# Optimization experiments

Measured on AMD Instinct MI355X. Metric: run time of the kernel, lower is better.

## Reference

```python
import jax, jax.numpy as jnp
import numpy as np

N_NODES = 50000
N_EDGES = 600000
IN_DIM = 128
HID = 128


def gcn_conv(x, W, b, src, dst, num_nodes):
    """PyG-style GCNConv: add self-loops, symmetric D^-1/2 (A+I) D^-1/2 normalization."""
    xw = x @ W  # [N, H]
    loop = jnp.arange(num_nodes)
    s = jnp.concatenate([src, loop])
    d = jnp.concatenate([dst, loop])
    deg = jax.ops.segment_sum(jnp.ones_like(d, dtype=xw.dtype), d, num_segments=num_nodes)
    dinv = jax.lax.rsqrt(deg)  # deg >= 1 thanks to self-loops
    norm = dinv[s] * dinv[d]  # [E+N]
    msgs = xw[s] * norm[:, None]  # gather + scale, [E+N, H]
    out = jax.ops.segment_sum(msgs, d, num_segments=num_nodes)
    return out + b


def setup_inputs() -> dict:
    key = jax.random.key(0)
    ks = jax.random.split(key, 12)
    sc_in = 1.0 / np.sqrt(IN_DIM)
    sc_h = 1.0 / np.sqrt(HID)
    sc_2h = 1.0 / np.sqrt(2 * HID)
    return {
        "x": jax.random.normal(ks[0], (N_NODES, IN_DIM), jnp.float32),
        "hidden_state": jax.random.normal(ks[1], (N_NODES, HID), jnp.float32),
        "edge_index": jax.random.randint(ks[2], (2, N_EDGES), 0, N_NODES, dtype=jnp.int32),
        "W_in": jax.random.normal(ks[3], (IN_DIM, HID), jnp.float32) * sc_in,
        "b_in": jnp.zeros((HID,), jnp.float32),
        "W_hid": jax.random.normal(ks[4], (HID, HID), jnp.float32) * sc_h,
        "b_hid": jnp.zeros((HID,), jnp.float32),
        "W_z": jax.random.normal(ks[5], (2 * HID, HID), jnp.float32) * sc_2h,
        "b_z": jnp.zeros((HID,), jnp.float32),
        "W_r": jax.random.normal(ks[6], (2 * HID, HID), jnp.float32) * sc_2h,
        "b_r": jnp.zeros((HID,), jnp.float32),
        "W_c": jax.random.normal(ks[7], (2 * HID, HID), jnp.float32) * sc_2h,
        "b_c": jnp.zeros((HID,), jnp.float32),
    }


def reference(x, hidden_state, edge_index, W_in, b_in, W_hid, b_hid, W_z, b_z, W_r, b_r, W_c, b_c):
    src, dst = edge_index[0], edge_index[1]
    n = x.shape[0]
    # two stacked GCN layers (dropout identity in eval mode)
    h1 = jax.nn.relu(gcn_conv(x, W_in, b_in, src, dst, n))
    emb = gcn_conv(h1, W_hid, b_hid, src, dst, n)  # [N, H]
    # GRU-style gating
    combined = jnp.concatenate([emb, hidden_state], axis=1)  # [N, 2H]
    update = jax.nn.sigmoid(combined @ W_z + b_z)
    reset = jax.nn.sigmoid(combined @ W_r + b_r)
    cand_in = jnp.concatenate([emb, reset * hidden_state], axis=1)
    candidate = jnp.tanh(cand_in @ W_c + b_c)
    new_hidden = (1.0 - update) * hidden_state + update * candidate
    return new_hidden
```

## Files before the change

kernel.cpp:

```cpp
#include <hip/hip_runtime.h>
#include <cstdint>
#include <cstddef>

typedef unsigned short u16;
typedef unsigned int   u32;

typedef __bf16 bf8   __attribute__((ext_vector_type(8)));
typedef float  f32x4 __attribute__((ext_vector_type(4)));

__device__ __forceinline__ float b2f(u16 v) {
  union { u32 i; float f; } c; c.i = ((u32)v) << 16; return c.f;
}
__device__ __forceinline__ u16 f2b(float f) {
  union { u32 i; float f; } c; c.f = f;
  u32 x = c.i;
  u32 r = (x + 0x7FFFu + ((x >> 16) & 1u)) >> 16;
  return (u16)r;
}
__device__ __forceinline__ float sigf(float x) { return 1.0f / (1.0f + __expf(-x)); }
__device__ __forceinline__ float tanhfast(float x) { return 2.0f * sigf(2.0f * x) - 1.0f; }

__device__ __forceinline__ bf8 cvt8(const float* __restrict__ p) {
  f32x4 lo = *(const f32x4*)p;
  f32x4 hi = *(const f32x4*)(p + 4);
  union { u16 s[8]; bf8 v; } c;
#pragma unroll
  for (int i = 0; i < 4; ++i) { c.s[i] = f2b(lo[i]); c.s[4 + i] = f2b(hi[i]); }
  return c.v;
}

__device__ __forceinline__ void ld_lds16(const u16* g, u16* l) {
  __builtin_amdgcn_global_load_lds((const __attribute__((address_space(1))) void*)g,
                                   (__attribute__((address_space(3))) void*)l, 16, 0, 0);
}

#define CSR_STRIDE 80

__global__ __launch_bounds__(256) void k_transpose(
    const float* __restrict__ W0, const float* __restrict__ W1,
    const float* __restrict__ W2, const float* __restrict__ W3,
    const float* __restrict__ W4,
    u16* __restrict__ B0, u16* __restrict__ B1, u16* __restrict__ B2,
    u16* __restrict__ B3, u16* __restrict__ B4,
    int* __restrict__ cnt, int N) {
  if (blockIdx.x >= 64) {
    int i = (blockIdx.x - 64) * 256 + threadIdx.x;
    if (i < N) cnt[i] = 0;
    return;
  }
  int t = blockIdx.x * 256 + threadIdx.x;
  const float* in; u16* out; int f;
  if (t < 2048)       { in = W0; out = B0; f = t; }
  else if (t < 4096)  { in = W1; out = B1; f = t - 2048; }
  else if (t < 8192)  { in = W2; out = B2; f = t - 4096; }
  else if (t < 12288) { in = W3; out = B3; f = t - 8192; }
  else                { in = W4; out = B4; f = t - 12288; }
  int ln = f & 15, quad = (f >> 4) & 3, c = (f >> 6) & 7, ks = (f >> 9) & 3, hh = f >> 11;
  int n = c * 16 + ln;
  int k0 = hh * 128 + ks * 32 + quad * 8;
  union { u16 s[8]; uint4 q; } tmp;
#pragma unroll
  for (int j = 0; j < 8; ++j) tmp.s[j] = f2b(in[(size_t)(k0 + j) * 128 + n]);
  *(uint4*)(out + (size_t)f * 8) = tmp.q;
}

__global__ void k_fill(const int* __restrict__ src, const int* __restrict__ dst,
                       int* __restrict__ cnt, int* __restrict__ csr, int E) {
  int e = blockIdx.x * 256 + threadIdx.x;
  if (e < E) {
    int d = dst[e];
    int pos = atomicAdd(&cnt[d], 1);
    if (pos < CSR_STRIDE) csr[(size_t)d * CSR_STRIDE + pos] = src[e];
  }
}

__global__ __launch_bounds__(256) void k_agg(const u16* __restrict__ y,
                                             const int* __restrict__ cnt,
                                             const int* __restrict__ csr,
                                             const float* __restrict__ bias,
                                             u16* __restrict__ out, int relu, int N) {
  int wv = (blockIdx.x * 256 + threadIdx.x) >> 6;
  int lane = threadIdx.x & 63;
  if (wv >= N) return;
  int g = lane >> 4, t = lane & 15;
  const uint4* yq = (const uint4*)y;
  int deg = cnt[wv];
  int degc = (deg < 64) ? deg : 64;
  long base = (long)wv * CSR_STRIDE;
  int myidx = (lane < degc) ? csr[base + lane] : 0;

  float a[8];
#pragma unroll
  for (int j = 0; j < 8; ++j) a[j] = 0.0f;

  for (int b = 0; b < degc; b += 8) {
    int e0 = b + g, e1 = b + 4 + g;
    int s0 = __shfl(myidx, (e0 < degc) ? e0 : 0, 64);
    int s1 = __shfl(myidx, (e1 < degc) ? e1 : 0, 64);
    uint4 v0 = yq[(size_t)s0 * 16 + t];
    uint4 v1 = yq[(size_t)s1 * 16 + t];
    if (e0 < degc) {
      const u32* w = (const u32*)&v0;
#pragma unroll
      for (int i = 0; i < 4; ++i) { a[2*i] += b2f((u16)(w[i] & 0xFFFF)); a[2*i+1] += b2f((u16)(w[i] >> 16)); }
    }
    if (e1 < degc) {
      const u32* w = (const u32*)&v1;
#pragma unroll
      for (int i = 0; i < 4; ++i) { a[2*i] += b2f((u16)(w[i] & 0xFFFF)); a[2*i+1] += b2f((u16)(w[i] >> 16)); }
    }
  }
#pragma unroll
  for (int j = 0; j < 8; ++j) {
    a[j] += __shfl_xor(a[j], 16, 64);
    a[j] += __shfl_xor(a[j], 32, 64);
  }
  if (g == 0) {
    int degt = (deg < CSR_STRIDE) ? deg : CSR_STRIDE;
    for (int p = 64; p < degt; ++p) {
      int s = csr[base + p];
      uint4 v = yq[(size_t)s * 16 + t];
      const u32* w = (const u32*)&v;
#pragma unroll
      for (int i = 0; i < 4; ++i) { a[2*i] += b2f((u16)(w[i] & 0xFFFF)); a[2*i+1] += b2f((u16)(w[i] >> 16)); }
    }
    uint4 sv = yq[(size_t)wv * 16 + t];
    const u32* w = (const u32*)&sv;
#pragma unroll
    for (int i = 0; i < 4; ++i) { a[2*i] += b2f((u16)(w[i] & 0xFFFF)); a[2*i+1] += b2f((u16)(w[i] >> 16)); }
    float di = rsqrtf((float)deg + 1.0f);
    f32x4 b0 = *(const f32x4*)(bias + t * 8);
    f32x4 b1 = *(const f32x4*)(bias + t * 8 + 4);
    union { u16 s[8]; uint4 q; } o;
#pragma unroll
    for (int j = 0; j < 8; ++j) {
      float r = di * a[j] + ((j < 4) ? b0[j] : b1[j - 4]);
      if (relu) r = fmaxf(r, 0.0f);
      o.s[j] = f2b(r);
    }
    ((uint4*)out)[(size_t)wv * 16 + t] = o.q;
  }
}

template <bool AF>
__global__ __launch_bounds__(256) void k_gemm(
    const void* __restrict__ Av,
    const u16* __restrict__ Bt,
    const int* __restrict__ cnt,
    u16* __restrict__ outb, int M) {
  __shared__ __align__(16) u16 bs[16384];
  int tid = threadIdx.x;
  int lane = tid & 63, wave = tid >> 6;
  int ln = lane & 15, quad = lane >> 4;
  int rowbase = blockIdx.x * 64 + wave * 16;
  int rowA = rowbase + ln;
  long rA = (rowA < M) ? rowA : (M - 1);

  {
    const u16* g = Bt + wave * 4096 + lane * 8;
    u16* l = bs + wave * 4096;
#pragma unroll
    for (int i = 0; i < 8; ++i) ld_lds16(g + i * 512, l + i * 512);
  }

  bf8 af[4];
#pragma unroll
  for (int ks = 0; ks < 4; ++ks) {
    int kk = ks * 32 + quad * 8;
    if (AF) af[ks] = cvt8((const float*)Av + rA * 128 + kk);
    else    af[ks] = *(const bf8*)((const u16*)Av + rA * 128 + kk);
  }

  f32x4 acc[8];
#pragma unroll
  for (int c = 0; c < 8; ++c) { acc[c][0] = 0.f; acc[c][1] = 0.f; acc[c][2] = 0.f; acc[c][3] = 0.f; }

  __syncthreads();
#pragma unroll
  for (int ks = 0; ks < 4; ++ks) {
#pragma unroll
    for (int c = 0; c < 8; ++c) {
      bf8 bfr = *(const bf8*)(bs + ks * 4096 + c * 512 + lane * 8);
      acc[c] = __builtin_amdgcn_mfma_f32_16x16x32_bf16(af[ks], bfr, acc[c], 0, 0, 0);
    }
  }

  int rb = rowbase + quad * 4;
  float rs[4];
#pragma unroll
  for (int r = 0; r < 4; ++r) {
    int row = rb + r;
    rs[r] = (row < M) ? rsqrtf((float)cnt[row] + 1.0f) : 0.0f;
  }
#pragma unroll
  for (int c = 0; c < 8; ++c) {
    int col = c * 16 + ln;
#pragma unroll
    for (int r = 0; r < 4; ++r) {
      int row = rb + r;
      if (row < M) outb[(size_t)row * 128 + col] = f2b(acc[c][r] * rs[r]);
    }
  }
}

__global__ __launch_bounds__(256, 2) void k_gru(
    const u16* __restrict__ emb, const float* __restrict__ h,
    const u16* __restrict__ Btz, const u16* __restrict__ Btr, const u16* __restrict__ Btc,
    const float* __restrict__ bz, const float* __restrict__ br, const float* __restrict__ bc,
    float* __restrict__ out, int M) {
  __shared__ __align__(16) u16 lds[32768];
  u16* const at = lds + 24576;
  int tid = threadIdx.x;
  int lane = tid & 63, wave = tid >> 6;
  int ln = lane & 15, quad = lane >> 4;
  int rowbase = blockIdx.x * 64 + wave * 16;
  int rowA = rowbase + ln;
  long rA = (rowA < M) ? rowA : (M - 1);
  int rb = rowbase + quad * 4;

  auto stage_zr = [&](int k, int s) {
#pragma unroll
    for (int i = 0; i < 2; ++i) {
      int off = (wave * 2 + i) * 512;
      ld_lds16(Btz + k * 4096 + off + lane * 8, &lds[s * 8192 + off]);
      ld_lds16(Btr + k * 4096 + off + lane * 8, &lds[s * 8192 + 4096 + off]);
    }
  };
  auto stage_c = [&](int k, int s) {
#pragma unroll
    for (int i = 0; i < 2; ++i) {
      int off = (wave * 2 + i) * 512;
      ld_lds16(Btc + k * 4096 + off + lane * 8, &lds[s * 4096 + off]);
    }
  };

  stage_zr(0, 0);
  stage_zr(1, 1);

  bf8 af_e[4], af_h[4];
#pragma unroll
  for (int ks = 0; ks < 4; ++ks)
    af_e[ks] = *(const bf8*)(emb + rA * 128 + ks * 32 + quad * 8);
#pragma unroll
  for (int ks = 0; ks < 4; ++ks)
    af_h[ks] = cvt8(h + rA * 128 + ks * 32 + quad * 8);

  f32x4 accz[8], accr[8];
#pragma unroll
  for (int c = 0; c < 8; ++c) {
    accz[c][0] = 0.f; accz[c][1] = 0.f; accz[c][2] = 0.f; accz[c][3] = 0.f;
    accr[c][0] = 0.f; accr[c][1] = 0.f; accr[c][2] = 0.f; accr[c][3] = 0.f;
  }

#pragma unroll
  for (int k = 0; k < 8; ++k) {
    if (k < 7) asm volatile("s_waitcnt vmcnt(4)\n\ts_barrier" ::: "memory");
    else       asm volatile("s_waitcnt vmcnt(0)\n\ts_barrier" ::: "memory");
    if (k < 6) stage_zr(k + 2, (k + 2) % 3);
    bf8 af = (k < 4) ? af_e[k] : af_h[k - 4];
    int s = k % 3;
#pragma unroll
    for (int c = 0; c < 8; ++c) {
      bf8 bz_ = *(const bf8*)(&lds[s * 8192 + (c * 64 + lane) * 8]);
      bf8 br_ = *(const bf8*)(&lds[s * 8192 + 4096 + (c * 64 + lane) * 8]);
      accz[c] = __builtin_amdgcn_mfma_f32_16x16x32_bf16(af, bz_, accz[c], 0, 0, 0);
      accr[c] = __builtin_amdgcn_mfma_f32_16x16x32_bf16(af, br_, accr[c], 0, 0, 0);
    }
  }

  stage_c(0, 0);
  stage_c(1, 1);

  f32x4 hc[8];
#pragma unroll
  for (int c = 0; c < 8; ++c) {
    int col = c * 16 + ln;
#pragma unroll
    for (int r = 0; r < 4; ++r) {
      int row = rb + r;
      hc[c][r] = (row < M) ? h[(size_t)row * 128 + col] : 0.0f;
    }
  }

#pragma unroll
  for (int c = 0; c < 8; ++c) {
    int col = c * 16 + ln;
    float bzc = bz[col], brc = br[col];
#pragma unroll
    for (int r = 0; r < 4; ++r) {
      float uu = sigf(accz[c][r] + bzc);
      float rr = sigf(accr[c][r] + brc);
      accz[c][r] = uu;
      int lrow = wave * 16 + quad * 4 + r;
      at[lrow * 128 + col] = f2b(rr * hc[c][r]);
      accr[c][r] = 0.0f;
    }
  }
  __syncthreads();

  bf8 af_at[4];
#pragma unroll
  for (int ks = 0; ks < 4; ++ks)
    af_at[ks] = *(const bf8*)(at + (wave * 16 + ln) * 128 + ks * 32 + quad * 8);

#pragma unroll
  for (int j = 0; j < 8; ++j) {
    if (j < 7) asm volatile("s_waitcnt vmcnt(2)\n\ts_barrier" ::: "memory");
    else       asm volatile("s_waitcnt vmcnt(0)\n\ts_barrier" ::: "memory");
    if (j < 6) stage_c(j + 2, (j + 2) % 3);
    bf8 af = (j < 4) ? af_e[j] : af_at[j - 4];
    int s = j % 3;
#pragma unroll
    for (int c = 0; c < 8; ++c) {
      bf8 bfr = *(const bf8*)(&lds[s * 4096 + (c * 64 + lane) * 8]);
      accr[c] = __builtin_amdgcn_mfma_f32_16x16x32_bf16(af, bfr, accr[c], 0, 0, 0);
    }
  }

#pragma unroll
  for (int c = 0; c < 8; ++c) {
    int col = c * 16 + ln;
    float bcc = bc[col];
#pragma unroll
    for (int r = 0; r < 4; ++r) {
      int row = rb + r;
      if (row < M) {
        float cd = tanhfast(accr[c][r] + bcc);
        float uu = accz[c][r];
        out[(size_t)row * 128 + col] = (1.0f - uu) * hc[c][r] + uu * cd;
      }
    }
  }
}

extern "C" void kernel_launch(void* const* d_in, const int* in_sizes, int n_in,
                              void* d_out, int out_size, void* d_ws, size_t ws_size,
                              hipStream_t stream) {
  const float* x     = (const float*)d_in[0];
  const float* h     = (const float*)d_in[1];
  const int*   ei    = (const int*)d_in[2];
  const float* W_in  = (const float*)d_in[3];
  const float* b_in  = (const float*)d_in[4];
  const float* W_hid = (const float*)d_in[5];
  const float* b_hid = (const float*)d_in[6];
  const float* W_z   = (const float*)d_in[7];
  const float* b_z   = (const float*)d_in[8];
  const float* W_r   = (const float*)d_in[9];
  const float* b_r   = (const float*)d_in[10];
  const float* W_c   = (const float*)d_in[11];
  const float* b_c   = (const float*)d_in[12];

  const int N = in_sizes[0] / 128;
  const int E = in_sizes[2] / 2;
  const int* src = ei;
  const int* dst = ei + E;

  char* p = (char*)d_ws;
  auto carve = [&](size_t bytes) { char* r = p; p += (bytes + 255) & ~(size_t)255; return r; };
  u16* Bt_in   = (u16*)carve((size_t)16384 * 2);
  u16* Bt_hid  = (u16*)carve((size_t)16384 * 2);
  u16* Bt_z    = (u16*)carve((size_t)32768 * 2);
  u16* Bt_r    = (u16*)carve((size_t)32768 * 2);
  u16* Bt_c    = (u16*)carve((size_t)32768 * 2);
  int* cnt  = (int*)carve((size_t)N * 4);
  int* csr  = (int*)carve((size_t)N * CSR_STRIDE * 4);
  u16* y    = (u16*)carve((size_t)N * 128 * 2);
  u16* h1   = (u16*)carve((size_t)N * 128 * 2);
  u16* emb  = (u16*)carve((size_t)N * 128 * 2);

  int gN = (N + 255) / 256;
  int gE = (E + 255) / 256;
  int gG = (N + 63) / 64;
  int gA = (N + 3) / 4;

  k_transpose<<<64 + gN, 256, 0, stream>>>(W_in, W_hid, W_z, W_r, W_c,
                                           Bt_in, Bt_hid, Bt_z, Bt_r, Bt_c, cnt, N);
  k_fill<<<gE, 256, 0, stream>>>(src, dst, cnt, csr, E);

  k_gemm<true><<<gG, 256, 0, stream>>>(x, Bt_in, cnt, y, N);
  k_agg<<<gA, 256, 0, stream>>>(y, cnt, csr, b_in, h1, 1, N);
  k_gemm<false><<<gG, 256, 0, stream>>>(h1, Bt_hid, cnt, y, N);
  k_agg<<<gA, 256, 0, stream>>>(y, cnt, csr, b_hid, emb, 0, N);
  k_gru<<<gG, 256, 0, stream>>>(emb, h, Bt_z, Bt_r, Bt_c, b_z, b_r, b_c, (float*)d_out, N);
}
```

Baseline: 255.5 us.

## Process 32 rows per wave in GRU kernel to reuse staged weights

Each wave in the GRU kernel now handles two 16-row fragments, so each 128-row block reuses every weight tile staged in LDS across twice as many MFMAs and the grid is halved. The reset-times-hidden tile is now written to a per-wave LDS region with an XOR swizzle, which removes the block-wide __syncthreads and avoids bank conflicts. The hidden state is re-read from global memory instead of being held in registers. Together these double accumulator registers and raise LDS use, which may lower occupancy under the 256,2 launch bounds.

```diff
diff --git a/kernel.cpp b/kernel.cpp
--- a/kernel.cpp
+++ b/kernel.cpp
@@ -208,15 +208,12 @@
     const u16* __restrict__ Btz, const u16* __restrict__ Btr, const u16* __restrict__ Btc,
     const float* __restrict__ bz, const float* __restrict__ br, const float* __restrict__ bc,
     float* __restrict__ out, int M) {
-  __shared__ __align__(16) u16 lds[32768];
-  u16* const at = lds + 24576;
+  __shared__ __align__(16) u16 lds[40960];
   int tid = threadIdx.x;
   int lane = tid & 63, wave = tid >> 6;
   int ln = lane & 15, quad = lane >> 4;
-  int rowbase = blockIdx.x * 64 + wave * 16;
-  int rowA = rowbase + ln;
-  long rA = (rowA < M) ? rowA : (M - 1);
-  int rb = rowbase + quad * 4;
+  int rowbase = blockIdx.x * 128 + wave * 32;
+  u16* const atw = lds + 24576 + wave * 4096;
 
   auto stage_zr = [&](int k, int s) {
 #pragma unroll
@@ -234,100 +231,117 @@
     }
   };
 
+  long rA0 = (rowbase + ln      < M) ? (rowbase + ln)      : (M - 1);
+  long rA1 = (rowbase + 16 + ln < M) ? (rowbase + 16 + ln) : (M - 1);
+
+  bf8 af_e[2][4], af_h[2][4];
+#pragma unroll
+  for (int ks = 0; ks < 4; ++ks) {
+    af_e[0][ks] = *(const bf8*)(emb + rA0 * 128 + ks * 32 + quad * 8);
+    af_e[1][ks] = *(const bf8*)(emb + rA1 * 128 + ks * 32 + quad * 8);
+  }
+#pragma unroll
+  for (int ks = 0; ks < 4; ++ks) {
+    af_h[0][ks] = cvt8(h + rA0 * 128 + ks * 32 + quad * 8);
+    af_h[1][ks] = cvt8(h + rA1 * 128 + ks * 32 + quad * 8);
+  }
+
   stage_zr(0, 0);
   stage_zr(1, 1);
 
-  bf8 af_e[4], af_h[4];
-#pragma unroll
-  for (int ks = 0; ks < 4; ++ks)
-    af_e[ks] = *(const bf8*)(emb + rA * 128 + ks * 32 + quad * 8);
-#pragma unroll
-  for (int ks = 0; ks < 4; ++ks)
-    af_h[ks] = cvt8(h + rA * 128 + ks * 32 + quad * 8);
-
-  f32x4 accz[8], accr[8];
-#pragma unroll
-  for (int c = 0; c < 8; ++c) {
-    accz[c][0] = 0.f; accz[c][1] = 0.f; accz[c][2] = 0.f; accz[c][3] = 0.f;
-    accr[c][0] = 0.f; accr[c][1] = 0.f; accr[c][2] = 0.f; accr[c][3] = 0.f;
-  }
+  f32x4 accz[2][8], accr[2][8];
+#pragma unroll
+  for (int rf = 0; rf < 2; ++rf)
+#pragma unroll
+    for (int c = 0; c < 8; ++c) {
+      accz[rf][c][0]=0.f; accz[rf][c][1]=0.f; accz[rf][c][2]=0.f; accz[rf][c][3]=0.f;
+      accr[rf][c][0]=0.f; accr[rf][c][1]=0.f; accr[rf][c][2]=0.f; accr[rf][c][3]=0.f;
+    }
 
 #pragma unroll
   for (int k = 0; k < 8; ++k) {
-    if (k < 7) asm volatile("s_waitcnt vmcnt(4)\n\ts_barrier" ::: "memory");
-    else       asm volatile("s_waitcnt vmcnt(0)\n\ts_barrier" ::: "memory");
+    if (k == 0 || k == 7) asm volatile("s_waitcnt vmcnt(0)\n\ts_barrier" ::: "memory");
+    else                  asm volatile("s_waitcnt vmcnt(4)\n\ts_barrier" ::: "memory");
     if (k < 6) stage_zr(k + 2, (k + 2) % 3);
-    bf8 af = (k < 4) ? af_e[k] : af_h[k - 4];
+    bf8 af0 = (k < 4) ? af_e[0][k] : af_h[0][k - 4];
+    bf8 af1 = (k < 4) ? af_e[1][k] : af_h[1][k - 4];
     int s = k % 3;
 #pragma unroll
     for (int c = 0; c < 8; ++c) {
       bf8 bz_ = *(const bf8*)(&lds[s * 8192 + (c * 64 + lane) * 8]);
       bf8 br_ = *(const bf8*)(&lds[s * 8192 + 4096 + (c * 64 + lane) * 8]);
-      accz[c] = __builtin_amdgcn_mfma_f32_16x16x32_bf16(af, bz_, accz[c], 0, 0, 0);
-      accr[c] = __builtin_amdgcn_mfma_f32_16x16x32_bf16(af, br_, accr[c], 0, 0, 0);
+      accz[0][c] = __builtin_amdgcn_mfma_f32_16x16x32_bf16(af0, bz_, accz[0][c], 0, 0, 0);
+      accz[1][c] = __builtin_amdgcn_mfma_f32_16x16x32_bf16(af1, bz_, accz[1][c], 0, 0, 0);
+      accr[0][c] = __builtin_amdgcn_mfma_f32_16x16x32_bf16(af0, br_, accr[0][c], 0, 0, 0);
+      accr[1][c] = __builtin_amdgcn_mfma_f32_16x16x32_bf16(af1, br_, accr[1][c], 0, 0, 0);
     }
   }
 
   stage_c(0, 0);
   stage_c(1, 1);
 
-  f32x4 hc[8];
-#pragma unroll
-  for (int c = 0; c < 8; ++c) {
-    int col = c * 16 + ln;
-#pragma unroll
-    for (int r = 0; r < 4; ++r) {
-      int row = rb + r;
-      hc[c][r] = (row < M) ? h[(size_t)row * 128 + col] : 0.0f;
-    }
-  }
-
-#pragma unroll
-  for (int c = 0; c < 8; ++c) {
-    int col = c * 16 + ln;
-    float bzc = bz[col], brc = br[col];
-#pragma unroll
-    for (int r = 0; r < 4; ++r) {
-      float uu = sigf(accz[c][r] + bzc);
-      float rr = sigf(accr[c][r] + brc);
-      accz[c][r] = uu;
-      int lrow = wave * 16 + quad * 4 + r;
-      at[lrow * 128 + col] = f2b(rr * hc[c][r]);
-      accr[c][r] = 0.0f;
-    }
-  }
-  __syncthreads();
-
-  bf8 af_at[4];
-#pragma unroll
-  for (int ks = 0; ks < 4; ++ks)
-    af_at[ks] = *(const bf8*)(at + (wave * 16 + ln) * 128 + ks * 32 + quad * 8);
+#pragma unroll
+  for (int rf = 0; rf < 2; ++rf) {
+#pragma unroll
+    for (int c = 0; c < 8; ++c) {
+      int col = c * 16 + ln;
+      float bzc = bz[col], brc = br[col];
+#pragma unroll
+      for (int r = 0; r < 4; ++r) {
+        int wl  = rf * 16 + quad * 4 + r;
+        int row = rowbase + wl;
+        float hcv = (row < M) ? h[(size_t)row * 128 + col] : 0.0f;
+        float uu = sigf(accz[rf][c][r] + bzc);
+        float rr = sigf(accr[rf][c][r] + brc);
+        accz[rf][c][r] = uu;
+        int idx = (wl * 128 + col) ^ ((wl & 7) << 3);
+        atw[idx] = f2b(rr * hcv);
+        accr[rf][c][r] = 0.0f;
+      }
+    }
+  }
+
+  bf8 af_at[2][4];
+#pragma unroll
+  for (int rf = 0; rf < 2; ++rf)
+#pragma unroll
+    for (int ks = 0; ks < 4; ++ks) {
+      int wl = rf * 16 + ln;
+      int idx = (wl * 128 + ks * 32 + quad * 8) ^ ((wl & 7) << 3);
+      af_at[rf][ks] = *(const bf8*)(&atw[idx]);
+    }
 
 #pragma unroll
   for (int j = 0; j < 8; ++j) {
-    if (j < 7) asm volatile("s_waitcnt vmcnt(2)\n\ts_barrier" ::: "memory");
-    else       asm volatile("s_waitcnt vmcnt(0)\n\ts_barrier" ::: "memory");
+    if (j == 0 || j == 7) asm volatile("s_waitcnt vmcnt(0)\n\ts_barrier" ::: "memory");
+    else                  asm volatile("s_waitcnt vmcnt(2)\n\ts_barrier" ::: "memory");
     if (j < 6) stage_c(j + 2, (j + 2) % 3);
-    bf8 af = (j < 4) ? af_e[j] : af_at[j - 4];
+    bf8 af0 = (j < 4) ? af_e[0][j] : af_at[0][j - 4];
+    bf8 af1 = (j < 4) ? af_e[1][j] : af_at[1][j - 4];
     int s = j % 3;
 #pragma unroll
     for (int c = 0; c < 8; ++c) {
       bf8 bfr = *(const bf8*)(&lds[s * 4096 + (c * 64 + lane) * 8]);
-      accr[c] = __builtin_amdgcn_mfma_f32_16x16x32_bf16(af, bfr, accr[c], 0, 0, 0);
-    }
-  }
-
-#pragma unroll
-  for (int c = 0; c < 8; ++c) {
-    int col = c * 16 + ln;
-    float bcc = bc[col];
-#pragma unroll
-    for (int r = 0; r < 4; ++r) {
-      int row = rb + r;
-      if (row < M) {
-        float cd = tanhfast(accr[c][r] + bcc);
-        float uu = accz[c][r];
-        out[(size_t)row * 128 + col] = (1.0f - uu) * hc[c][r] + uu * cd;
+      accr[0][c] = __builtin_amdgcn_mfma_f32_16x16x32_bf16(af0, bfr, accr[0][c], 0, 0, 0);
+      accr[1][c] = __builtin_amdgcn_mfma_f32_16x16x32_bf16(af1, bfr, accr[1][c], 0, 0, 0);
+    }
+  }
+
+#pragma unroll
+  for (int rf = 0; rf < 2; ++rf) {
+#pragma unroll
+    for (int c = 0; c < 8; ++c) {
+      int col = c * 16 + ln;
+      float bcc = bc[col];
+#pragma unroll
+      for (int r = 0; r < 4; ++r) {
+        int row = rowbase + rf * 16 + quad * 4 + r;
+        if (row < M) {
+          float hcv = h[(size_t)row * 128 + col];
+          float cd = tanhfast(accr[rf][c][r] + bcc);
+          float uu = accz[rf][c][r];
+          out[(size_t)row * 128 + col] = (1.0f - uu) * hcv + uu * cd;
+        }
       }
     }
   }
@@ -371,6 +385,7 @@
   int gN = (N + 255) / 256;
   int gE = (E + 255) / 256;
   int gG = (N + 63) / 64;
+  int gGru = (N + 127) / 128;
   int gA = (N + 3) / 4;
 
   k_transpose<<<64 + gN, 256, 0, stream>>>(W_in, W_hid, W_z, W_r, W_c,
@@ -381,5 +396,5 @@
   k_agg<<<gA, 256, 0, stream>>>(y, cnt, csr, b_in, h1, 1, N);
   k_gemm<false><<<gG, 256, 0, stream>>>(h1, Bt_hid, cnt, y, N);
   k_agg<<<gA, 256, 0, stream>>>(y, cnt, csr, b_hid, emb, 0, N);
-  k_gru<<<gG, 256, 0, stream>>>(emb, h, Bt_z, Bt_r, Bt_c, b_z, b_r, b_c, (float*)d_out, N);
-}
+  k_gru<<<gGru, 256, 0, stream>>>(emb, h, Bt_z, Bt_r, Bt_c, b_z, b_r, b_c, (float*)d_out, N);
+}
```

Measured after the change: 270.6 us. 5.9% more time.

## Shrink GRU kernel LDS footprint to raise occupancy, split z/r staging

Applied to the files above, without the earlier changes.

Cuts LDS use of the GRU gating kernel from 64KB to 40KB by staging the z and r weight tiles as separate 16-step pipeline stages instead of paired 8-step stages. Launch bounds are raised to 4 blocks per CU. The reset-times-hidden tile moves into a per-wave, XOR-swizzled region so the block-wide sync before reading it can be dropped and LDS bank conflicts reduced. The trade-off is twice as many barriers in the z/r loop and more register pressure under the tighter launch bound, which could cause spills.

```diff
diff --git a/kernel.cpp b/kernel.cpp
--- a/kernel.cpp
+++ b/kernel.cpp
@@ -203,13 +203,12 @@
   }
 }
 
-__global__ __launch_bounds__(256, 2) void k_gru(
+__global__ __launch_bounds__(256, 4) void k_gru(
     const u16* __restrict__ emb, const float* __restrict__ h,
     const u16* __restrict__ Btz, const u16* __restrict__ Btr, const u16* __restrict__ Btc,
     const float* __restrict__ bz, const float* __restrict__ br, const float* __restrict__ bc,
     float* __restrict__ out, int M) {
-  __shared__ __align__(16) u16 lds[32768];
-  u16* const at = lds + 24576;
+  __shared__ __align__(16) u16 lds[20480];
   int tid = threadIdx.x;
   int lane = tid & 63, wave = tid >> 6;
   int ln = lane & 15, quad = lane >> 4;
@@ -217,13 +216,14 @@
   int rowA = rowbase + ln;
   long rA = (rowA < M) ? rowA : (M - 1);
   int rb = rowbase + quad * 4;
-
-  auto stage_zr = [&](int k, int s) {
+  u16* const atw = lds + 12288 + wave * 2048;
+
+  auto stage_zr = [&](int t, int s) {
+    const u16* src = ((t & 1) ? Btr : Btz) + (t >> 1) * 4096;
 #pragma unroll
     for (int i = 0; i < 2; ++i) {
       int off = (wave * 2 + i) * 512;
-      ld_lds16(Btz + k * 4096 + off + lane * 8, &lds[s * 8192 + off]);
-      ld_lds16(Btr + k * 4096 + off + lane * 8, &lds[s * 8192 + 4096 + off]);
+      ld_lds16(src + off + lane * 8, &lds[s * 4096 + off]);
     }
   };
   auto stage_c = [&](int k, int s) {
@@ -234,17 +234,17 @@
     }
   };
 
+  bf8 af_e[4], af_h[4];
+#pragma unroll
+  for (int ks = 0; ks < 4; ++ks)
+    af_e[ks] = *(const bf8*)(emb + rA * 128 + ks * 32 + quad * 8);
+#pragma unroll
+  for (int ks = 0; ks < 4; ++ks)
+    af_h[ks] = cvt8(h + rA * 128 + ks * 32 + quad * 8);
+
   stage_zr(0, 0);
   stage_zr(1, 1);
 
-  bf8 af_e[4], af_h[4];
-#pragma unroll
-  for (int ks = 0; ks < 4; ++ks)
-    af_e[ks] = *(const bf8*)(emb + rA * 128 + ks * 32 + quad * 8);
-#pragma unroll
-  for (int ks = 0; ks < 4; ++ks)
-    af_h[ks] = cvt8(h + rA * 128 + ks * 32 + quad * 8);
-
   f32x4 accz[8], accr[8];
 #pragma unroll
   for (int c = 0; c < 8; ++c) {
@@ -253,23 +253,23 @@
   }
 
 #pragma unroll
-  for (int k = 0; k < 8; ++k) {
-    if (k < 7) asm volatile("s_waitcnt vmcnt(4)\n\ts_barrier" ::: "memory");
-    else       asm volatile("s_waitcnt vmcnt(0)\n\ts_barrier" ::: "memory");
-    if (k < 6) stage_zr(k + 2, (k + 2) % 3);
-    bf8 af = (k < 4) ? af_e[k] : af_h[k - 4];
-    int s = k % 3;
+  for (int t = 0; t < 16; ++t) {
+    if (t < 15) asm volatile("s_waitcnt vmcnt(2)\n\ts_barrier" ::: "memory");
+    else        asm volatile("s_waitcnt vmcnt(0)\n\ts_barrier" ::: "memory");
+    if (t < 14) stage_zr(t + 2, (t + 2) % 3);
+    int ks = t >> 1;
+    bf8 af = (ks < 4) ? af_e[ks] : af_h[ks - 4];
+    int s = t % 3;
+    f32x4* acc = (t & 1) ? accr : accz;
 #pragma unroll
     for (int c = 0; c < 8; ++c) {
-      bf8 bz_ = *(const bf8*)(&lds[s * 8192 + (c * 64 + lane) * 8]);
-      bf8 br_ = *(const bf8*)(&lds[s * 8192 + 4096 + (c * 64 + lane) * 8]);
-      accz[c] = __builtin_amdgcn_mfma_f32_16x16x32_bf16(af, bz_, accz[c], 0, 0, 0);
-      accr[c] = __builtin_amdgcn_mfma_f32_16x16x32_bf16(af, br_, accr[c], 0, 0, 0);
-    }
-  }
-
-  stage_c(0, 0);
-  stage_c(1, 1);
+      bf8 bfr = *(const bf8*)(&lds[s * 4096 + (c * 64 + lane) * 8]);
+      acc[c] = __builtin_amdgcn_mfma_f32_16x16x32_bf16(af, bfr, acc[c], 0, 0, 0);
+    }
+  }
+
+  stage_c(0, 1);
+  stage_c(1, 2);
 
   f32x4 hc[8];
 #pragma unroll
@@ -291,25 +291,27 @@
       float uu = sigf(accz[c][r] + bzc);
       float rr = sigf(accr[c][r] + brc);
       accz[c][r] = uu;
-      int lrow = wave * 16 + quad * 4 + r;
-      at[lrow * 128 + col] = f2b(rr * hc[c][r]);
+      int wl = quad * 4 + r;
+      int idx = (wl * 128 + col) ^ ((wl & 7) << 3);
+      atw[idx] = f2b(rr * hc[c][r]);
       accr[c][r] = 0.0f;
     }
   }
-  __syncthreads();
-
   bf8 af_at[4];
 #pragma unroll
-  for (int ks = 0; ks < 4; ++ks)
-    af_at[ks] = *(const bf8*)(at + (wave * 16 + ln) * 128 + ks * 32 + quad * 8);
+  for (int ks = 0; ks < 4; ++ks) {
+    int wl = ln;
+    int idx = (wl * 128 + ks * 32 + quad * 8) ^ ((wl & 7) << 3);
+    af_at[ks] = *(const bf8*)(&atw[idx]);
+  }
 
 #pragma unroll
   for (int j = 0; j < 8; ++j) {
     if (j < 7) asm volatile("s_waitcnt vmcnt(2)\n\ts_barrier" ::: "memory");
     else       asm volatile("s_waitcnt vmcnt(0)\n\ts_barrier" ::: "memory");
-    if (j < 6) stage_c(j + 2, (j + 2) % 3);
+    if (j < 6) stage_c(j + 2, j % 3);
     bf8 af = (j < 4) ? af_e[j] : af_at[j - 4];
-    int s = j % 3;
+    int s = (j + 1) % 3;
 #pragma unroll
     for (int c = 0; c < 8; ++c) {
       bf8 bfr = *(const bf8*)(&lds[s * 4096 + (c * 64 + lane) * 8]);
```

Result: slower. 280.2 us (+9.6%).
